# Optimization experiments

Hardware: AMD Instinct MI355X
Metric: run time of the kernel (lower is better)

The kernel has to match this reference:

```python
import jax, jax.numpy as jnp
import numpy as np
from jax import lax

F_, W_, H_ = -0.01, -0.1, 1.0
K5 = np.array([[F_]*5, [F_, W_, W_, W_, F_], [F_, W_, H_, W_, F_], [F_, W_, W_, W_, F_], [F_]*5], dtype=np.float32)
K3 = np.array([[W_, W_, W_], [W_, H_, W_], [W_, W_, W_]], dtype=np.float32)


def depthwise_conv(x, k2d):
    # x: [B,C,H,W]; same small kernel applied independently to every channel
    C = x.shape[1]
    kh = k2d.shape[0]
    kernel = jnp.broadcast_to(jnp.asarray(k2d, x.dtype)[None, None], (C, 1, kh, kh))
    pad = kh // 2
    return lax.conv_general_dilated(
        x, kernel,
        window_strides=(1, 1),
        padding=[(pad, pad), (pad, pad)],
        dimension_numbers=("NCHW", "OIHW", "NCHW"),
        feature_group_count=C,
    )


def maxpool5(x):
    # kernel_size=5, stride=1, padding=2 (torch MaxPool2d pads with -inf)
    return lax.reduce_window(
        x, -jnp.inf, lax.max,
        window_dimensions=(1, 1, 5, 5),
        window_strides=(1, 1, 1, 1),
        padding=[(0, 0), (0, 0), (2, 2), (2, 2)],
    )


def setup_inputs() -> dict:
    key = jax.random.key(0)
    x = jax.random.normal(key, (8, 64, 256, 256), dtype=jnp.float32)
    return {"x": x}


def reference(x):
    edge = depthwise_conv(x, K5) + depthwise_conv(x, K3)
    return jnp.abs(maxpool5(edge))
```

## Files before the change

kernel.cpp:

```cpp
#include <hip/hip_runtime.h>
#include <math.h>


#define TY 32
#define STEPS (TY + 8)

typedef float vfloat4 __attribute__((ext_vector_type(4)));

__global__ __launch_bounds__(256, 2)
void edgepool_kernel(const float* __restrict__ xin, float* __restrict__ yout) {
    const int lane  = threadIdx.x & 63;
    const int wave  = threadIdx.x >> 6;
    const int blk   = blockIdx.x;
    const int plane = blk >> 1;
    const int strip = ((blk & 1) << 2) | wave;
    const int y0    = strip * TY;

    const float4* __restrict__ in4  = (const float4*)xin + (size_t)plane * 16384;
    vfloat4*      __restrict__ out4 = (vfloat4*)    yout + (size_t)plane * 16384;

    const float Wa = -0.01f, Wb = -0.19f, Wc = 2.2f;
    const float NINF = -INFINITY;

    float Cr[3][4];
    float P5[5][4];
    float Q3[4][4];
    float M5[5][4];
#pragma unroll
    for (int j = 0; j < 4; ++j) {
        Cr[0][j] = Cr[1][j] = Cr[2][j] = 0.f;
        Q3[0][j] = Q3[1][j] = Q3[2][j] = Q3[3][j] = 0.f;
        P5[0][j] = P5[1][j] = P5[2][j] = P5[3][j] = P5[4][j] = 0.f;
        M5[0][j] = M5[1][j] = M5[2][j] = M5[3][j] = M5[4][j] = NINF;
    }

#pragma unroll
    for (int t = 0; t < STEPS; ++t) {
        const int  r   = y0 - 4 + t;
        const bool rin = (unsigned)r < 256u;
        const int  rc  = rin ? r : (r < 0 ? 0 : 255);
        const float4 vv = in4[rc * 64 + lane];
        const float v0 = rin ? vv.x : 0.f;
        const float v1 = rin ? vv.y : 0.f;
        const float v2 = rin ? vv.z : 0.f;
        const float v3 = rin ? vv.w : 0.f;

        float lm2 = __shfl(v2, lane - 1, 64);
        float lm1 = __shfl(v3, lane - 1, 64);
        float rp0 = __shfl(v0, lane + 1, 64);
        float rp1 = __shfl(v1, lane + 1, 64);
        lm2 = (lane == 0)  ? 0.f : lm2;
        lm1 = (lane == 0)  ? 0.f : lm1;
        rp0 = (lane == 63) ? 0.f : rp0;
        rp1 = (lane == 63) ? 0.f : rp1;

        const float h3_0 = lm1 + v0 + v1;
        const float h3_1 = v0 + v1 + v2;
        const float h3_2 = v1 + v2 + v3;
        const float h3_3 = v2 + v3 + rp0;
        const float h5_0 = lm2 + lm1 + v0 + v1 + v2;
        const float h5_1 = lm1 + v0 + v1 + v2 + v3;
        const float h5_2 = v0 + v1 + v2 + v3 + rp0;
        const float h5_3 = v1 + v2 + v3 + rp0 + rp1;

        const int tc = t % 3, tp = t % 5, tq = t % 4;
        Cr[tc][0] = v0;   Cr[tc][1] = v1;   Cr[tc][2] = v2;   Cr[tc][3] = v3;
        P5[tp][0] = h5_0; P5[tp][1] = h5_1; P5[tp][2] = h5_2; P5[tp][3] = h5_3;
        Q3[tq][0] = h3_0; Q3[tq][1] = h3_1; Q3[tq][2] = h3_2; Q3[tq][3] = h3_3;

        const int  er  = r - 2;
        const bool ein = (unsigned)er < 256u;
        const int a1 = (t + 4) % 5, a2 = (t + 3) % 5, a3 = (t + 2) % 5, a4 = (t + 1) % 5;
        const int b1 = (t + 3) % 4, b2 = (t + 2) % 4, b3 = (t + 1) % 4;
        const int cc = (t + 1) % 3;
        float e[4];
#pragma unroll
        for (int j = 0; j < 4; ++j) {
            const float S5 = P5[tp][j] + P5[a1][j] + P5[a2][j] + P5[a3][j] + P5[a4][j];
            const float S3 = Q3[b1][j] + Q3[b2][j] + Q3[b3][j];
            const float ev = fmaf(Wc, Cr[cc][j], fmaf(Wb, S3, Wa * S5));
            e[j] = ein ? ev : NINF;
        }

        float el2 = __shfl(e[2], lane - 1, 64);
        float el1 = __shfl(e[3], lane - 1, 64);
        float er0 = __shfl(e[0], lane + 1, 64);
        float er1 = __shfl(e[1], lane + 1, 64);
        el2 = (lane == 0)  ? NINF : el2;
        el1 = (lane == 0)  ? NINF : el1;
        er0 = (lane == 63) ? NINF : er0;
        er1 = (lane == 63) ? NINF : er1;

        M5[tp][0] = fmaxf(fmaxf(fmaxf(el2, el1), fmaxf(e[0], e[1])), e[2]);
        M5[tp][1] = fmaxf(fmaxf(fmaxf(el1, e[0]), fmaxf(e[1], e[2])), e[3]);
        M5[tp][2] = fmaxf(fmaxf(fmaxf(e[0], e[1]), fmaxf(e[2], e[3])), er0);
        M5[tp][3] = fmaxf(fmaxf(fmaxf(e[1], e[2]), fmaxf(e[3], er0)), er1);

        if (t >= 8) {
            const int o = r - 4;
            vfloat4 ov;
            ov.x = fabsf(fmaxf(fmaxf(fmaxf(M5[0][0], M5[1][0]), fmaxf(M5[2][0], M5[3][0])), M5[4][0]));
            ov.y = fabsf(fmaxf(fmaxf(fmaxf(M5[0][1], M5[1][1]), fmaxf(M5[2][1], M5[3][1])), M5[4][1]));
            ov.z = fabsf(fmaxf(fmaxf(fmaxf(M5[0][2], M5[1][2]), fmaxf(M5[2][2], M5[3][2])), M5[4][2]));
            ov.w = fabsf(fmaxf(fmaxf(fmaxf(M5[0][3], M5[1][3]), fmaxf(M5[2][3], M5[3][3])), M5[4][3]));
            __builtin_nontemporal_store(ov, &out4[o * 64 + lane]);
        }
    }
}

extern "C" void kernel_launch(void* const* d_in, const int* in_sizes, int n_in,
                              void* d_out, int out_size, void* d_ws, size_t ws_size,
                              hipStream_t stream) {
    const float* x   = (const float*)d_in[0];
    float*       out = (float*)d_out;
    hipLaunchKernelGGL(edgepool_kernel, dim3(1024), dim3(256), 0, stream, x, out);
}
```

Measured before the change: 235.9 us.

## Halve strip height, raise occupancy, and shrink rolling register buffers

Each wave now covers a 16-row strip instead of 32, with twice as many blocks launched and the launch bound raised to 8 blocks per SM. This exposes more parallelism and latency hiding. The rolling center and 3-row buffers are shortened by reading them before overwriting, and the horizontal sums now share partial terms to save adds. The cost is that halo rows (8 per strip) become a larger fraction of the rows loaded and computed, so redundant work increases.

```diff
diff --git a/kernel.cpp b/kernel.cpp
--- a/kernel.cpp
+++ b/kernel.cpp
@@ -2,18 +2,18 @@
 #include <math.h>
 
 
-#define TY 32
+#define TY 16
 #define STEPS (TY + 8)
 
 typedef float vfloat4 __attribute__((ext_vector_type(4)));
 
-__global__ __launch_bounds__(256, 2)
+__global__ __launch_bounds__(256, 8)
 void edgepool_kernel(const float* __restrict__ xin, float* __restrict__ yout) {
     const int lane  = threadIdx.x & 63;
     const int wave  = threadIdx.x >> 6;
     const int blk   = blockIdx.x;
-    const int plane = blk >> 1;
-    const int strip = ((blk & 1) << 2) | wave;
+    const int plane = blk >> 2;
+    const int strip = ((blk & 3) << 2) | wave;
     const int y0    = strip * TY;
 
     const float4* __restrict__ in4  = (const float4*)xin + (size_t)plane * 16384;
@@ -22,14 +22,14 @@
     const float Wa = -0.01f, Wb = -0.19f, Wc = 2.2f;
     const float NINF = -INFINITY;
 
-    float Cr[3][4];
+    float Cr[2][4];
     float P5[5][4];
-    float Q3[4][4];
+    float Q3[3][4];
     float M5[5][4];
 #pragma unroll
     for (int j = 0; j < 4; ++j) {
-        Cr[0][j] = Cr[1][j] = Cr[2][j] = 0.f;
-        Q3[0][j] = Q3[1][j] = Q3[2][j] = Q3[3][j] = 0.f;
+        Cr[0][j] = Cr[1][j] = 0.f;
+        Q3[0][j] = Q3[1][j] = Q3[2][j] = 0.f;
         P5[0][j] = P5[1][j] = P5[2][j] = P5[3][j] = P5[4][j] = 0.f;
         M5[0][j] = M5[1][j] = M5[2][j] = M5[3][j] = M5[4][j] = NINF;
     }
@@ -54,25 +54,25 @@
         rp0 = (lane == 63) ? 0.f : rp0;
         rp1 = (lane == 63) ? 0.f : rp1;
 
-        const float h3_0 = lm1 + v0 + v1;
-        const float h3_1 = v0 + v1 + v2;
-        const float h3_2 = v1 + v2 + v3;
-        const float h3_3 = v2 + v3 + rp0;
-        const float h5_0 = lm2 + lm1 + v0 + v1 + v2;
-        const float h5_1 = lm1 + v0 + v1 + v2 + v3;
-        const float h5_2 = v0 + v1 + v2 + v3 + rp0;
-        const float h5_3 = v1 + v2 + v3 + rp0 + rp1;
+        const float s01  = v0 + v1;
+        const float s23  = v2 + v3;
+        const float h3_0 = lm1 + s01;
+        const float h3_1 = s01 + v2;
+        const float h3_2 = v1 + s23;
+        const float h3_3 = s23 + rp0;
+        const float h5_0 = lm2 + h3_0 + v2;
+        const float h5_1 = lm1 + s01 + s23;
+        const float h5_2 = s01 + s23 + rp0;
+        const float h5_3 = v1 + s23 + rp0 + rp1;
 
-        const int tc = t % 3, tp = t % 5, tq = t % 4;
-        Cr[tc][0] = v0;   Cr[tc][1] = v1;   Cr[tc][2] = v2;   Cr[tc][3] = v3;
+        const int tp = t % 5;
         P5[tp][0] = h5_0; P5[tp][1] = h5_1; P5[tp][2] = h5_2; P5[tp][3] = h5_3;
-        Q3[tq][0] = h3_0; Q3[tq][1] = h3_1; Q3[tq][2] = h3_2; Q3[tq][3] = h3_3;
 
         const int  er  = r - 2;
         const bool ein = (unsigned)er < 256u;
         const int a1 = (t + 4) % 5, a2 = (t + 3) % 5, a3 = (t + 2) % 5, a4 = (t + 1) % 5;
-        const int b1 = (t + 3) % 4, b2 = (t + 2) % 4, b3 = (t + 1) % 4;
-        const int cc = (t + 1) % 3;
+        const int b1 = (t + 2) % 3, b2 = (t + 1) % 3, b3 = t % 3;
+        const int cc = t % 2;
         float e[4];
 #pragma unroll
         for (int j = 0; j < 4; ++j) {
@@ -81,6 +81,9 @@
             const float ev = fmaf(Wc, Cr[cc][j], fmaf(Wb, S3, Wa * S5));
             e[j] = ein ? ev : NINF;
         }
+
+        Q3[b3][0] = h3_0; Q3[b3][1] = h3_1; Q3[b3][2] = h3_2; Q3[b3][3] = h3_3;
+        Cr[cc][0] = v0;   Cr[cc][1] = v1;   Cr[cc][2] = v2;   Cr[cc][3] = v3;
 
         float el2 = __shfl(e[2], lane - 1, 64);
         float el1 = __shfl(e[3], lane - 1, 64);
@@ -113,5 +116,5 @@
                               hipStream_t stream) {
     const float* x   = (const float*)d_in[0];
     float*       out = (float*)d_out;
-    hipLaunchKernelGGL(edgepool_kernel, dim3(1024), dim3(256), 0, stream, x, out);
+    hipLaunchKernelGGL(edgepool_kernel, dim3(2048), dim3(256), 0, stream, x, out);
 }
```

Result: slower. 561.6 us (+138.1%).
